# Kernel tuning notes

Hardware: AMD Instinct MI355X
Metric: run time of the kernel (lower is better)

## Reference

```python
import jax, jax.numpy as jnp
import numpy as np

N_EMBD = 1024
N_HEAD = 16


def setup_inputs() -> dict:
    key = jax.random.key(0)
    ks = jax.random.split(key, 5)
    C = N_EMBD
    x = jax.random.normal(ks[0], (4, 2048, C), dtype=jnp.float32)
    s = 1.0 / np.sqrt(C)
    W_attn = jax.random.normal(ks[1], (C, 3 * C), dtype=jnp.float32) * s
    b_attn = jnp.zeros((3 * C,), dtype=jnp.float32)
    W_proj = jax.random.normal(ks[2], (C, C), dtype=jnp.float32) * s
    b_proj = jnp.zeros((C,), dtype=jnp.float32)
    return {"x": x, "W_attn": W_attn, "b_attn": b_attn, "W_proj": W_proj, "b_proj": b_proj}


def reference(x, W_attn, b_attn, W_proj, b_proj):
    B, T, C = x.shape
    H = N_HEAD
    D = C // H
    qkv = x @ W_attn + b_attn                      # [B,T,3C]
    q, k, v = jnp.split(qkv, 3, axis=-1)
    # [B,H,T,D]
    q = q.reshape(B, T, H, D).transpose(0, 2, 1, 3)
    k = k.reshape(B, T, H, D).transpose(0, 2, 1, 3)
    v = v.reshape(B, T, H, D).transpose(0, 2, 1, 3)
    scale = 1.0 / jnp.sqrt(jnp.asarray(D, dtype=x.dtype))
    att = jnp.einsum('bhqd,bhkd->bhqk', q, k) * scale   # [B,H,T,T]
    causal = jnp.tril(jnp.ones((T, T), dtype=bool))
    att = jnp.where(causal, att, jnp.finfo(att.dtype).min)
    att = jax.nn.softmax(att, axis=-1)
    y = jnp.einsum('bhqk,bhkd->bhqd', att, v)            # [B,H,T,D]
    y = y.transpose(0, 2, 1, 3).reshape(B, T, C)
    return y @ W_proj + b_proj
```

## Files before the change

kernel.cpp:

```cpp
#include <hip/hip_runtime.h>
#include <type_traits>

typedef __attribute__((ext_vector_type(8))) short short8;
typedef __attribute__((ext_vector_type(8))) unsigned short ushort8;
typedef __attribute__((ext_vector_type(4))) float floatx4;

__device__ __forceinline__ unsigned short f2bf(float f) {
    union { float f; unsigned int i; } v;
    v.f = f;
    unsigned int u = v.i;
    unsigned int r = (u + 0x7FFFu + ((u >> 16) & 1u)) >> 16;
    return (unsigned short)r;
}

__device__ __forceinline__ void gload_lds16(const unsigned short* g, unsigned short* lds_base) {
    __builtin_amdgcn_global_load_lds(
        (const __attribute__((address_space(1))) unsigned int*)g,
        (__attribute__((address_space(3))) unsigned int*)lds_base,
        16, 0, 0);
}

__global__ __launch_bounds__(256) void cvt_f32_bf16_kernel(
    const float* __restrict__ src, unsigned short* __restrict__ dst, int n8)
{
    int i = blockIdx.x * 256 + threadIdx.x;
    if (i >= n8) return;
    const float4* s = (const float4*)src + (size_t)i * 2;
    float4 a = s[0];
    float4 b = s[1];
    ushort8 r;
    r[0] = f2bf(a.x); r[1] = f2bf(a.y); r[2] = f2bf(a.z); r[3] = f2bf(a.w);
    r[4] = f2bf(b.x); r[5] = f2bf(b.y); r[6] = f2bf(b.z); r[7] = f2bf(b.w);
    *((ushort8*)dst + i) = r;
}

__global__ __launch_bounds__(256) void transpose_cvt_kernel(
    const float* __restrict__ src, unsigned short* __restrict__ dst, int K, int N)
{
    __shared__ float tile[32][33];
    const int tx = threadIdx.x & 31;
    const int ty = threadIdx.x >> 5;
    const int k0 = blockIdx.y * 32, n0 = blockIdx.x * 32;
#pragma unroll
    for (int i = 0; i < 4; ++i)
        tile[ty + i * 8][tx] = src[(size_t)(k0 + ty + i * 8) * N + n0 + tx];
    __syncthreads();
#pragma unroll
    for (int i = 0; i < 4; ++i)
        dst[(size_t)(n0 + ty + i * 8) * K + k0 + tx] = f2bf(tile[tx][ty + i * 8]);
}

template <int MODE, typename OutT>
__global__ __launch_bounds__(256) void gemm128_kernel(
    const unsigned short* __restrict__ A,
    const unsigned short* __restrict__ Bt,
    const float* __restrict__ bias,
    OutT* __restrict__ C,
    unsigned short* __restrict__ Qo,
    unsigned short* __restrict__ Ko,
    unsigned short* __restrict__ Vto,
    int M, int N, int K)
{
    __shared__ __align__(16) unsigned short As[128 * 32];
    __shared__ __align__(16) unsigned short Bs[128 * 32];

    const int tid  = threadIdx.x;
    const int lane = tid & 63;
    const int w    = tid >> 6;
    const int wm   = w & 1;
    const int wn   = w >> 1;
    const int quad = lane >> 4;
    const int l16  = lane & 15;

    const int m0 = blockIdx.y * 128;
    const int n0 = blockIdx.x * 128;

    floatx4 acc[4][4];
#pragma unroll
    for (int i = 0; i < 4; ++i)
#pragma unroll
        for (int j = 0; j < 4; ++j) acc[i][j] = (floatx4)0.0f;

    const int r0 = tid >> 2;
    const int kc = (((tid & 3) ^ ((tid >> 3) & 3)) << 3);
    const unsigned short* Ag = A  + (size_t)(m0 + r0) * K + kc;
    const unsigned short* Bg = Bt + (size_t)(n0 + r0) * K + kc;
    unsigned short* AsW = As + w * 512;
    unsigned short* BsW = Bs + w * 512;

    const int sw = ((quad ^ ((l16 >> 1) & 3)) << 3);

    for (int k0 = 0; k0 < K; k0 += 32) {
        __syncthreads();
#pragma unroll
        for (int i = 0; i < 2; ++i) {
            gload_lds16(Ag + (size_t)(i * 64) * K + k0, AsW + i * 2048);
            gload_lds16(Bg + (size_t)(i * 64) * K + k0, BsW + i * 2048);
        }
        __syncthreads();

        short8 a[4], b[4];
#pragma unroll
        for (int mi = 0; mi < 4; ++mi)
            a[mi] = *(const short8*)&As[(wm * 64 + mi * 16 + l16) * 32 + sw];
#pragma unroll
        for (int ni = 0; ni < 4; ++ni)
            b[ni] = *(const short8*)&Bs[(wn * 64 + ni * 16 + l16) * 32 + sw];
#pragma unroll
        for (int mi = 0; mi < 4; ++mi)
#pragma unroll
            for (int ni = 0; ni < 4; ++ni)
                acc[mi][ni] = __builtin_amdgcn_mfma_f32_16x16x32_bf16(a[mi], b[ni], acc[mi][ni], 0, 0, 0);
    }

#pragma unroll
    for (int ni = 0; ni < 4; ++ni) {
        const int n = n0 + wn * 64 + ni * 16 + l16;
        const float bval = bias[n];
        const int seg = n >> 10;
        const int nl  = n & 1023;
#pragma unroll
        for (int mi = 0; mi < 4; ++mi) {
            if constexpr (MODE == 0) {
#pragma unroll
                for (int r = 0; r < 4; ++r) {
                    const int m = m0 + wm * 64 + mi * 16 + (quad << 2) + r;
                    const float val = acc[mi][ni][r] + bval;
                    if constexpr (std::is_same<OutT, unsigned short>::value)
                        C[(size_t)m * N + n] = f2bf(val);
                    else
                        C[(size_t)m * N + n] = val;
                }
            } else {
                if (seg < 2) {
                    unsigned short* P = (seg == 0) ? Qo : Ko;
#pragma unroll
                    for (int r = 0; r < 4; ++r) {
                        const int m = m0 + wm * 64 + mi * 16 + (quad << 2) + r;
                        P[(size_t)m * 1024 + nl] = f2bf(acc[mi][ni][r] + bval);
                    }
                } else {
                    const int mb = m0 + wm * 64 + mi * 16 + (quad << 2);
                    const int bb = mb >> 11, t0 = mb & 2047;
                    unsigned int lo = (unsigned int)f2bf(acc[mi][ni][0] + bval) |
                                      ((unsigned int)f2bf(acc[mi][ni][1] + bval) << 16);
                    unsigned int hi = (unsigned int)f2bf(acc[mi][ni][2] + bval) |
                                      ((unsigned int)f2bf(acc[mi][ni][3] + bval) << 16);
                    uint2 pv; pv.x = lo; pv.y = hi;
                    *(uint2*)(Vto + ((size_t)bb * 1024 + nl) * 2048 + t0) = pv;
                }
            }
        }
    }
}

__global__ __launch_bounds__(256, 8) void attn_kernel(
    const unsigned short* __restrict__ Q,
    const unsigned short* __restrict__ Kq,
    const unsigned short* __restrict__ Vt,
    unsigned short* __restrict__ Y)
{
    const int T = 2048;

    int idx = blockIdx.x;
    int qt  = 31 - (idx >> 6);
    int bh  = idx & 63;
    int b   = bh >> 4;
    int h   = bh & 15;

    const int tid  = threadIdx.x;
    const int lane = tid & 63;
    const int w    = tid >> 6;
    const int quad = lane >> 4;
    const int l16  = lane & 15;

    __shared__ __align__(16) unsigned short Ks2[8 * 64 * 8];
    __shared__ __align__(16) unsigned short Vs2[8 * 64 * 8];
    __shared__ __align__(16) unsigned short Ps[4][16][72];

    const unsigned short* qp =
        Q + (size_t)(b * T + qt * 64 + (w << 4) + l16) * 1024 + h * 64;
    short8 qf0 = *(const short8*)(qp + (quad << 3));
    short8 qf1 = *(const short8*)(qp + 32 + (quad << 3));

    float l_run = 0.0f;
    floatx4 o[4];
#pragma unroll
    for (int ns = 0; ns < 4; ++ns) o[ns] = (floatx4)0.0f;

    const unsigned short* kg0p = Kq + (size_t)(b * T + lane) * 1024 + h * 64 + (w) * 8;
    const unsigned short* kg1p = Kq + (size_t)(b * T + lane) * 1024 + h * 64 + (w + 4) * 8;
    const unsigned short* vg0p = Vt + ((size_t)(b * 1024 + h * 64 + lane)) * 2048 + (w) * 8;
    const unsigned short* vg1p = Vt + ((size_t)(b * 1024 + h * 64 + lane)) * 2048 + (w + 4) * 8;

    const int qg_local = (w << 4) + l16;

    const float SC2 = 0.18033688011112042f;
    const float MB2 = -17.312340490667562f;

    const int ktiles = qt + 1;
    for (int kt = 0; kt < ktiles; ++kt) {
        const int key0 = kt << 6;
        __syncthreads();
        gload_lds16(kg0p + (size_t)key0 * 1024, Ks2 + (w) * 512);
        gload_lds16(kg1p + (size_t)key0 * 1024, Ks2 + (w + 4) * 512);
        gload_lds16(vg0p + key0, Vs2 + (w) * 512);
        gload_lds16(vg1p + key0, Vs2 + (w + 4) * 512);
        __syncthreads();

        floatx4 s[4];
#pragma unroll
        for (int ks = 0; ks < 4; ++ks) {
            s[ks] = (floatx4)0.0f;
            short8 kf0 = *(const short8*)&Ks2[((0 * 4 + quad) * 64 + ks * 16 + l16) * 8];
            short8 kf1 = *(const short8*)&Ks2[((1 * 4 + quad) * 64 + ks * 16 + l16) * 8];
            s[ks] = __builtin_amdgcn_mfma_f32_16x16x32_bf16(kf0, qf0, s[ks], 0, 0, 0);
            s[ks] = __builtin_amdgcn_mfma_f32_16x16x32_bf16(kf1, qf1, s[ks], 0, 0, 0);
        }

        if (kt < qt) {
#pragma unroll
            for (int ks = 0; ks < 4; ++ks) {
                float pv0 = __builtin_amdgcn_exp2f(fmaf(s[ks][0], SC2, MB2));
                float pv1 = __builtin_amdgcn_exp2f(fmaf(s[ks][1], SC2, MB2));
                float pv2 = __builtin_amdgcn_exp2f(fmaf(s[ks][2], SC2, MB2));
                float pv3 = __builtin_amdgcn_exp2f(fmaf(s[ks][3], SC2, MB2));
                l_run += (pv0 + pv1) + (pv2 + pv3);
                unsigned int lo, hi;
                asm("v_cvt_pk_bf16_f32 %0, %1, %2" : "=v"(lo) : "v"(pv0), "v"(pv1));
                asm("v_cvt_pk_bf16_f32 %0, %1, %2" : "=v"(hi) : "v"(pv2), "v"(pv3));
                uint2 pk; pk.x = lo; pk.y = hi;
                *(uint2*)&Ps[w][l16][(ks << 4) + (quad << 2)] = pk;
            }
        } else {
            const int kq4 = quad << 2;
#pragma unroll
            for (int ks = 0; ks < 4; ++ks) {
                const int kb = (ks << 4) + kq4;
                float a0 = (kb + 0 <= qg_local) ? fmaf(s[ks][0], SC2, MB2) : -100000.0f;
                float a1 = (kb + 1 <= qg_local) ? fmaf(s[ks][1], SC2, MB2) : -100000.0f;
                float a2 = (kb + 2 <= qg_local) ? fmaf(s[ks][2], SC2, MB2) : -100000.0f;
                float a3 = (kb + 3 <= qg_local) ? fmaf(s[ks][3], SC2, MB2) : -100000.0f;
                float pv0 = __builtin_amdgcn_exp2f(a0);
                float pv1 = __builtin_amdgcn_exp2f(a1);
                float pv2 = __builtin_amdgcn_exp2f(a2);
                float pv3 = __builtin_amdgcn_exp2f(a3);
                l_run += (pv0 + pv1) + (pv2 + pv3);
                unsigned int lo, hi;
                asm("v_cvt_pk_bf16_f32 %0, %1, %2" : "=v"(lo) : "v"(pv0), "v"(pv1));
                asm("v_cvt_pk_bf16_f32 %0, %1, %2" : "=v"(hi) : "v"(pv2), "v"(pv3));
                uint2 pk; pk.x = lo; pk.y = hi;
                *(uint2*)&Ps[w][l16][(ks << 4) + (quad << 2)] = pk;
            }
        }

        short8 pf0 = *(const short8*)&Ps[w][l16][quad << 3];
        short8 pf1 = *(const short8*)&Ps[w][l16][32 + (quad << 3)];
#pragma unroll
        for (int ns = 0; ns < 4; ++ns) {
            short8 vf0 = *(const short8*)&Vs2[((0 * 4 + quad) * 64 + ns * 16 + l16) * 8];
            short8 vf1 = *(const short8*)&Vs2[((1 * 4 + quad) * 64 + ns * 16 + l16) * 8];
            o[ns] = __builtin_amdgcn_mfma_f32_16x16x32_bf16(pf0, vf0, o[ns], 0, 0, 0);
            o[ns] = __builtin_amdgcn_mfma_f32_16x16x32_bf16(pf1, vf1, o[ns], 0, 0, 0);
        }
    }

    float ssum = l_run;
    ssum += __shfl_xor(ssum, 16, 64);
    ssum += __shfl_xor(ssum, 32, 64);
    const float linv = 1.0f / ssum;
    float li[4];
#pragma unroll
    for (int r = 0; r < 4; ++r) li[r] = __shfl(linv, (quad << 2) + r, 64);

#pragma unroll
    for (int ns = 0; ns < 4; ++ns) {
        int d = (ns << 4) + l16;
#pragma unroll
        for (int r = 0; r < 4; ++r) {
            int t = qt * 64 + (w << 4) + (quad << 2) + r;
            Y[(size_t)(b * T + t) * 1024 + h * 64 + d] = f2bf(o[ns][r] * li[r]);
        }
    }
}

extern "C" void kernel_launch(void* const* d_in, const int* in_sizes, int n_in,
                              void* d_out, int out_size, void* d_ws, size_t ws_size,
                              hipStream_t stream) {
    const float* x  = (const float*)d_in[0];
    const float* Wa = (const float*)d_in[1];
    const float* ba = (const float*)d_in[2];
    const float* Wp = (const float*)d_in[3];
    const float* bp = (const float*)d_in[4];
    float* out = (float*)d_out;

    const size_t NX = (size_t)8192 * 1024;

    unsigned short* Qb  = (unsigned short*)d_ws;
    unsigned short* Kb  = Qb  + NX;
    unsigned short* Vtb = Kb  + NX;
    unsigned short* Yb  = Vtb + NX;
    unsigned short* xb  = Yb  + NX;
    unsigned short* Wat = xb  + NX;
    unsigned short* Wpt = Wat + (size_t)3072 * 1024;

    cvt_f32_bf16_kernel<<<(int)(NX / 8 / 256), 256, 0, stream>>>(x, xb, (int)(NX / 8));
    transpose_cvt_kernel<<<dim3(3072 / 32, 1024 / 32), 256, 0, stream>>>(Wa, Wat, 1024, 3072);
    transpose_cvt_kernel<<<dim3(1024 / 32, 1024 / 32), 256, 0, stream>>>(Wp, Wpt, 1024, 1024);

    gemm128_kernel<1, unsigned short><<<dim3(3072 / 128, 8192 / 128), 256, 0, stream>>>(
        xb, Wat, ba, (unsigned short*)nullptr, Qb, Kb, Vtb, 8192, 3072, 1024);

    attn_kernel<<<4 * 16 * (2048 / 64), 256, 0, stream>>>(Qb, Kb, Vtb, Yb);

    gemm128_kernel<0, float><<<dim3(1024 / 128, 8192 / 128), 256, 0, stream>>>(
        Yb, Wpt, bp, out, nullptr, nullptr, nullptr, 8192, 1024, 1024);
}
```

Baseline: 269.9 us.

## Double-buffer LDS tiles with async prefetch in GEMM and attention loops

Both the GEMM and the attention main loops now use two LDS buffers. The next tile's global-to-LDS loads are issued before computing on the current tile, with explicit vmcnt waits and raw barriers replacing the two __syncthreads per iteration. This is meant to hide global load latency behind MFMA work. It doubles LDS use per block, so attention launch bounds drop from 8 to 4 blocks per CU, which may reduce occupancy.

```diff
diff --git a/kernel.cpp b/kernel.cpp
--- a/kernel.cpp
+++ b/kernel.cpp
@@ -18,6 +18,12 @@
         (const __attribute__((address_space(1))) unsigned int*)g,
         (__attribute__((address_space(3))) unsigned int*)lds_base,
         16, 0, 0);
+}
+
+__device__ __forceinline__ void pbar() {
+    asm volatile("" ::: "memory");
+    __builtin_amdgcn_s_barrier();
+    asm volatile("" ::: "memory");
 }
 
 __global__ __launch_bounds__(256) void cvt_f32_bf16_kernel(
@@ -61,8 +67,8 @@
     unsigned short* __restrict__ Vto,
     int M, int N, int K)
 {
-    __shared__ __align__(16) unsigned short As[128 * 32];
-    __shared__ __align__(16) unsigned short Bs[128 * 32];
+    __shared__ __align__(16) unsigned short As[2][128 * 32];
+    __shared__ __align__(16) unsigned short Bs[2][128 * 32];
 
     const int tid  = threadIdx.x;
     const int lane = tid & 63;
@@ -85,33 +91,47 @@
     const int kc = (((tid & 3) ^ ((tid >> 3) & 3)) << 3);
     const unsigned short* Ag = A  + (size_t)(m0 + r0) * K + kc;
     const unsigned short* Bg = Bt + (size_t)(n0 + r0) * K + kc;
-    unsigned short* AsW = As + w * 512;
-    unsigned short* BsW = Bs + w * 512;
 
     const int sw = ((quad ^ ((l16 >> 1) & 3)) << 3);
 
-    for (int k0 = 0; k0 < K; k0 += 32) {
-        __syncthreads();
-#pragma unroll
-        for (int i = 0; i < 2; ++i) {
-            gload_lds16(Ag + (size_t)(i * 64) * K + k0, AsW + i * 2048);
-            gload_lds16(Bg + (size_t)(i * 64) * K + k0, BsW + i * 2048);
-        }
-        __syncthreads();
-
-        short8 a[4], b[4];
+    const int nt = K >> 5;
+
+#define STAGE(buf, t)                                                          \
+    do {                                                                       \
+        const int kk = (t) << 5;                                               \
+        gload_lds16(Ag + kk,                    &As[buf][w * 512]);            \
+        gload_lds16(Ag + (size_t)64 * K + kk,   &As[buf][w * 512 + 2048]);     \
+        gload_lds16(Bg + kk,                    &Bs[buf][w * 512]);            \
+        gload_lds16(Bg + (size_t)64 * K + kk,   &Bs[buf][w * 512 + 2048]);     \
+    } while (0)
+
+    STAGE(0, 0);
+
+    for (int t = 0; t < nt; ++t) {
+        const int b = t & 1;
+        if (t + 1 < nt) {
+            STAGE(b ^ 1, t + 1);
+            asm volatile("s_waitcnt vmcnt(4)" ::: "memory");
+        } else {
+            asm volatile("s_waitcnt vmcnt(0)" ::: "memory");
+        }
+        pbar();
+
+        short8 a[4], bb[4];
 #pragma unroll
         for (int mi = 0; mi < 4; ++mi)
-            a[mi] = *(const short8*)&As[(wm * 64 + mi * 16 + l16) * 32 + sw];
+            a[mi] = *(const short8*)&As[b][(wm * 64 + mi * 16 + l16) * 32 + sw];
 #pragma unroll
         for (int ni = 0; ni < 4; ++ni)
-            b[ni] = *(const short8*)&Bs[(wn * 64 + ni * 16 + l16) * 32 + sw];
+            bb[ni] = *(const short8*)&Bs[b][(wn * 64 + ni * 16 + l16) * 32 + sw];
 #pragma unroll
         for (int mi = 0; mi < 4; ++mi)
 #pragma unroll
             for (int ni = 0; ni < 4; ++ni)
-                acc[mi][ni] = __builtin_amdgcn_mfma_f32_16x16x32_bf16(a[mi], b[ni], acc[mi][ni], 0, 0, 0);
+                acc[mi][ni] = __builtin_amdgcn_mfma_f32_16x16x32_bf16(a[mi], bb[ni], acc[mi][ni], 0, 0, 0);
+        pbar();
     }
+#undef STAGE
 
 #pragma unroll
     for (int ni = 0; ni < 4; ++ni) {
@@ -141,20 +161,20 @@
                     }
                 } else {
                     const int mb = m0 + wm * 64 + mi * 16 + (quad << 2);
-                    const int bb = mb >> 11, t0 = mb & 2047;
+                    const int bbk = mb >> 11, t0 = mb & 2047;
                     unsigned int lo = (unsigned int)f2bf(acc[mi][ni][0] + bval) |
                                       ((unsigned int)f2bf(acc[mi][ni][1] + bval) << 16);
                     unsigned int hi = (unsigned int)f2bf(acc[mi][ni][2] + bval) |
                                       ((unsigned int)f2bf(acc[mi][ni][3] + bval) << 16);
                     uint2 pv; pv.x = lo; pv.y = hi;
-                    *(uint2*)(Vto + ((size_t)bb * 1024 + nl) * 2048 + t0) = pv;
+                    *(uint2*)(Vto + ((size_t)bbk * 1024 + nl) * 2048 + t0) = pv;
                 }
             }
         }
     }
 }
 
-__global__ __launch_bounds__(256, 8) void attn_kernel(
+__global__ __launch_bounds__(256, 4) void attn_kernel(
     const unsigned short* __restrict__ Q,
     const unsigned short* __restrict__ Kq,
     const unsigned short* __restrict__ Vt,
@@ -174,8 +194,8 @@
     const int quad = lane >> 4;
     const int l16  = lane & 15;
 
-    __shared__ __align__(16) unsigned short Ks2[8 * 64 * 8];
-    __shared__ __align__(16) unsigned short Vs2[8 * 64 * 8];
+    __shared__ __align__(16) unsigned short Ks2[2][8 * 64 * 8];
+    __shared__ __align__(16) unsigned short Vs2[2][8 * 64 * 8];
     __shared__ __align__(16) unsigned short Ps[4][16][72];
 
     const unsigned short* qp =
@@ -199,21 +219,34 @@
     const float MB2 = -17.312340490667562f;
 
     const int ktiles = qt + 1;
+
+#define ASTAGE(buf, kt)                                                         \
+    do {                                                                        \
+        const int key0_ = (kt) << 6;                                            \
+        gload_lds16(kg0p + (size_t)key0_ * 1024, &Ks2[buf][(w) * 512]);         \
+        gload_lds16(kg1p + (size_t)key0_ * 1024, &Ks2[buf][(w + 4) * 512]);     \
+        gload_lds16(vg0p + key0_,                &Vs2[buf][(w) * 512]);         \
+        gload_lds16(vg1p + key0_,                &Vs2[buf][(w + 4) * 512]);     \
+    } while (0)
+
+    ASTAGE(0, 0);
+
     for (int kt = 0; kt < ktiles; ++kt) {
-        const int key0 = kt << 6;
-        __syncthreads();
-        gload_lds16(kg0p + (size_t)key0 * 1024, Ks2 + (w) * 512);
-        gload_lds16(kg1p + (size_t)key0 * 1024, Ks2 + (w + 4) * 512);
-        gload_lds16(vg0p + key0, Vs2 + (w) * 512);
-        gload_lds16(vg1p + key0, Vs2 + (w + 4) * 512);
-        __syncthreads();
+        const int bb = kt & 1;
+        if (kt + 1 < ktiles) {
+            ASTAGE(bb ^ 1, kt + 1);
+            asm volatile("s_waitcnt vmcnt(4)" ::: "memory");
+        } else {
+            asm volatile("s_waitcnt vmcnt(0)" ::: "memory");
+        }
+        pbar();
 
         floatx4 s[4];
 #pragma unroll
         for (int ks = 0; ks < 4; ++ks) {
             s[ks] = (floatx4)0.0f;
-            short8 kf0 = *(const short8*)&Ks2[((0 * 4 + quad) * 64 + ks * 16 + l16) * 8];
-            short8 kf1 = *(const short8*)&Ks2[((1 * 4 + quad) * 64 + ks * 16 + l16) * 8];
+            short8 kf0 = *(const short8*)&Ks2[bb][((0 * 4 + quad) * 64 + ks * 16 + l16) * 8];
+            short8 kf1 = *(const short8*)&Ks2[bb][((1 * 4 + quad) * 64 + ks * 16 + l16) * 8];
             s[ks] = __builtin_amdgcn_mfma_f32_16x16x32_bf16(kf0, qf0, s[ks], 0, 0, 0);
             s[ks] = __builtin_amdgcn_mfma_f32_16x16x32_bf16(kf1, qf1, s[ks], 0, 0, 0);
         }
@@ -258,12 +291,14 @@
         short8 pf1 = *(const short8*)&Ps[w][l16][32 + (quad << 3)];
 #pragma unroll
         for (int ns = 0; ns < 4; ++ns) {
-            short8 vf0 = *(const short8*)&Vs2[((0 * 4 + quad) * 64 + ns * 16 + l16) * 8];
-            short8 vf1 = *(const short8*)&Vs2[((1 * 4 + quad) * 64 + ns * 16 + l16) * 8];
+            short8 vf0 = *(const short8*)&Vs2[bb][((0 * 4 + quad) * 64 + ns * 16 + l16) * 8];
+            short8 vf1 = *(const short8*)&Vs2[bb][((1 * 4 + quad) * 64 + ns * 16 + l16) * 8];
             o[ns] = __builtin_amdgcn_mfma_f32_16x16x32_bf16(pf0, vf0, o[ns], 0, 0, 0);
             o[ns] = __builtin_amdgcn_mfma_f32_16x16x32_bf16(pf1, vf1, o[ns], 0, 0, 0);
         }
+        pbar();
     }
+#undef ASTAGE
 
     float ssum = l_run;
     ssum += __shfl_xor(ssum, 16, 64);
```

Measured after the change: 268.9 us. Within noise of the previous version (-0.3%).
